# Kernel tuning notes

Measured on AMD Instinct MI355X. Metric: run time of the kernel, lower is better.

The kernel has to match this reference:

```python
import jax, jax.numpy as jnp
import numpy as np
import math

N, S, D, C, CLASSES = 512, 256, 512, 1024, 1000


def setup_inputs() -> dict:
    key = jax.random.key(0)
    ks = jax.random.split(key, 9)
    q = jax.random.normal(ks[0], (N, D), dtype=jnp.float32)
    K = jax.random.normal(ks[1], (N, S, D), dtype=jnp.float32)
    V = jax.random.normal(ks[2], (N, S, D), dtype=jnp.float32)
    codebook = jax.random.normal(ks[3], (C, D), dtype=jnp.float32) / math.sqrt(D)
    Wq = jax.random.normal(ks[4], (D, D), dtype=jnp.float32) / math.sqrt(D)
    Wc = jax.random.normal(ks[5], (CLASSES, D), dtype=jnp.float32) / math.sqrt(D)
    bc = jnp.zeros((CLASSES,), dtype=jnp.float32)
    Wr = jax.random.normal(ks[6], (D, D), dtype=jnp.float32) / math.sqrt(D)
    br = jnp.zeros((D,), dtype=jnp.float32)
    return {"q": q, "K": K, "V": V, "codebook": codebook,
            "Wq": Wq, "Wc": Wc, "bc": bc, "Wr": Wr, "br": br}


def reference(q, K, V, codebook, Wq, Wc, bc, Wr, br):
    d = q.shape[-1]
    scale = math.sqrt(d)
    # query projection (Linear, no bias): q @ Wq^T
    q_proj = jnp.einsum('nd,ed->ne', q, Wq)
    # query-to-codebook soft assignment [n, c]
    code_weights = jax.nn.softmax(jnp.einsum('nd,cd->nc', q_proj, codebook) / scale, axis=-1)
    # slot-to-codebook soft assignment [n, s, c]
    slot_code_weights = jax.nn.softmax(jnp.einsum('nsd,cd->nsc', K, codebook) / scale, axis=-1)
    # fused: einsum('nc,ncd->nd', code_weights, einsum('nsc,nsd->ncd', ...))
    # == contract c first to get per-slot weights [n, s], then mix V.
    effective_weights = jnp.einsum('nc,nsc->ns', code_weights, slot_code_weights)
    summary = jnp.einsum('ns,nsd->nd', effective_weights, V)
    logits = jnp.einsum('nd,kd->nk', summary, Wc) + bc
    recon = jnp.einsum('nd,ed->ne', summary, Wr) + br
    return (logits, recon, effective_weights)
```

## Files before the change

kernel.cpp:

```cpp
#include <hip/hip_runtime.h>
#include <hip/hip_bf16.h>
#include <stdint.h>


typedef float  f32x4 __attribute__((ext_vector_type(4)));
typedef float  f32x2 __attribute__((ext_vector_type(2)));
typedef short  s16x8 __attribute__((ext_vector_type(8)));

__device__ __forceinline__ unsigned short f2bf(float x){
  unsigned u = __float_as_uint(x);
  u += 0x7fffu + ((u >> 16) & 1u);
  return (unsigned short)(u >> 16);
}
__device__ __forceinline__ float hsum4(f32x4 v){ return v[0]+v[1]+v[2]+v[3]; }

static constexpr float INV_SCALE = 0.04419417382415922f;

__global__ __launch_bounds__(256) void k_prep(const float* __restrict__ cb,
                                              unsigned short* __restrict__ cbB,
                                              const float* __restrict__ q,
                                              const float* __restrict__ Wq,
                                              float* __restrict__ cw){
  __shared__ __align__(16) float qrow[2][512];
  __shared__ __align__(16) float qproj[2][512];
  __shared__ float ev[2][1024];
  __shared__ float red[256];
  __shared__ float tot[2];
  const int t = threadIdx.x;

  if (blockIdx.x < 256){
    const int g = blockIdx.x*256 + t;
    const int ks8 = g & 3;
    const int cr  = (g >> 2) & 31;
    const int kk  = (g >> 7) & 15;
    const int p   = g >> 11;
    const int c = p*32 + cr;
    const int k = kk*32 + ks8*8;
    const float* src = cb + (size_t)c*512 + k;
    const f32x4 v0 = *(const f32x4*)(src);
    const f32x4 v1 = *(const f32x4*)(src + 4);
    s16x8 o;
    o[0]=(short)f2bf(v0[0]*INV_SCALE); o[1]=(short)f2bf(v0[1]*INV_SCALE);
    o[2]=(short)f2bf(v0[2]*INV_SCALE); o[3]=(short)f2bf(v0[3]*INV_SCALE);
    o[4]=(short)f2bf(v1[0]*INV_SCALE); o[5]=(short)f2bf(v1[1]*INV_SCALE);
    o[6]=(short)f2bf(v1[2]*INV_SCALE); o[7]=(short)f2bf(v1[3]*INV_SCALE);
    *(s16x8*)(cbB + (size_t)g*8) = o;
    return;
  }

  const int n0 = (blockIdx.x - 256)*2;
  #pragma unroll
  for (int j = 0; j < 4; ++j){
    const int o = t + 256*j; const int ni = o >> 9, d = o & 511;
    qrow[ni][d] = q[(size_t)(n0+ni)*512 + d];
  }
  __syncthreads();
  {
    const f32x4* q0 = (const f32x4*)qrow[0];
    const f32x4* q1 = (const f32x4*)qrow[1];
    #pragma unroll 1
    for (int j = 0; j < 2; ++j){
      const int e = t + 256*j;
      const f32x4* w4 = (const f32x4*)(Wq + (size_t)e*512);
      f32x4 a0={0,0,0,0},a1={0,0,0,0};
      for (int d = 0; d < 128; ++d){
        const f32x4 wv = w4[d];
        a0 += wv*q0[d]; a1 += wv*q1[d];
      }
      qproj[0][e]=hsum4(a0); qproj[1][e]=hsum4(a1);
    }
  }
  __syncthreads();
  {
    const f32x4* p0 = (const f32x4*)qproj[0];
    const f32x4* p1 = (const f32x4*)qproj[1];
    #pragma unroll 1
    for (int j = 0; j < 4; ++j){
      const int c = t + 256*j;
      const f32x4* c4 = (const f32x4*)(cb + (size_t)c*512);
      f32x4 a0={0,0,0,0},a1={0,0,0,0};
      for (int d = 0; d < 128; ++d){
        const f32x4 wv = c4[d];
        a0 += wv*p0[d]; a1 += wv*p1[d];
      }
      ev[0][c] = __expf(hsum4(a0)*INV_SCALE);
      ev[1][c] = __expf(hsum4(a1)*INV_SCALE);
    }
  }
  __syncthreads();
  for (int ni = 0; ni < 2; ++ni){
    red[t] = ev[ni][t] + ev[ni][t+256] + ev[ni][t+512] + ev[ni][t+768];
    __syncthreads();
    for (int off = 128; off > 0; off >>= 1){
      if (t < off) red[t] += red[t+off];
      __syncthreads();
    }
    if (t == 0) tot[ni] = red[0];
    __syncthreads();
  }
  #pragma unroll
  for (int j = 0; j < 8; ++j){
    const int o = t + 256*j; const int ni = o >> 10, c = o & 1023;
    cw[(size_t)(n0+ni)*1024 + c] = ev[ni][c] / tot[ni];
  }
}

template<bool FUSE_V>
__global__ __launch_bounds__(512, 4) void k_scores(const float* __restrict__ Kt,
                                                   const unsigned short* __restrict__ cbB,
                                                   const float* __restrict__ cw,
                                                   float* __restrict__ ew_out,
                                                   const float* __restrict__ Vp,
                                                   float* __restrict__ partial){
  __shared__ __align__(16) short sA[64*512];
  __shared__ float cwl[1024];
  __shared__ float pe[8][64];
  __shared__ float pw[8][64];
  __shared__ float ewl[64];

  const int t    = threadIdx.x;
  const int lane = t & 63;
  const int w    = t >> 6;
  const int m0   = blockIdx.x * 64;
  const int n    = m0 >> 8;

  {
    const int row = t >> 3;
    const float* src = Kt + (size_t)(m0 + row) * 512;
    #pragma unroll
    for (int j = 0; j < 8; ++j){
      const int slot = (t & 7) + 8*j;
      const f32x4 v0 = *(const f32x4*)(src + slot*8);
      const f32x4 v1 = *(const f32x4*)(src + slot*8 + 4);
      s16x8 o;
      o[0]=(short)f2bf(v0[0]); o[1]=(short)f2bf(v0[1]); o[2]=(short)f2bf(v0[2]); o[3]=(short)f2bf(v0[3]);
      o[4]=(short)f2bf(v1[0]); o[5]=(short)f2bf(v1[1]); o[6]=(short)f2bf(v1[2]); o[7]=(short)f2bf(v1[3]);
      const int sp = slot ^ (row & 7);
      *(s16x8*)&sA[row*512 + sp*8] = o;
    }
  }
  cwl[t]       = cw[(size_t)n*1024 + t];
  cwl[t + 512] = cw[(size_t)n*1024 + t + 512];
  __syncthreads();

  const int kg = lane >> 4;
  const int lr = lane & 15;
  const int rot = blockIdx.x & 3;

  float es[4][4], ws[4][4];
  #pragma unroll
  for (int fr = 0; fr < 4; ++fr)
    #pragma unroll
    for (int r = 0; r < 4; ++r){ es[fr][r] = 0.f; ws[fr][r] = 0.f; }

  #pragma unroll 1
  for (int p = 0; p < 4; ++p){
    const int ci = (p + rot) & 3;
    f32x4 acc[4][2];
    #pragma unroll
    for (int fr = 0; fr < 4; ++fr)
      #pragma unroll
      for (int fc = 0; fc < 2; ++fc) acc[fr][fc] = (f32x4){0.f,0.f,0.f,0.f};

    const unsigned short* pbase = cbB + ((size_t)(ci*8 + w))*16384;
    const int loff = lr*32 + kg*8;

    s16x8 a[4], b[2][2];
    #pragma unroll
    for (int fc = 0; fc < 2; ++fc)
      b[0][fc] = *(const s16x8*)(pbase + 0*1024 + fc*512 + loff);
    #pragma unroll
    for (int fc = 0; fc < 2; ++fc)
      b[1][fc] = *(const s16x8*)(pbase + 1*1024 + fc*512 + loff);

    #pragma unroll
    for (int kk = 0; kk < 16; ++kk){
      if (kk < 15) asm volatile("s_waitcnt vmcnt(2)" ::: "memory");
      else         asm volatile("s_waitcnt vmcnt(0)" ::: "memory");
      __builtin_amdgcn_sched_barrier(0);
      #pragma unroll
      for (int fr = 0; fr < 4; ++fr){
        const int row = fr*16 + lr;
        const int sp  = (kk*4 + kg) ^ (row & 7);
        a[fr] = *(const s16x8*)&sA[row*512 + sp*8];
      }
      __builtin_amdgcn_s_setprio(1);
      #pragma unroll
      for (int fr = 0; fr < 4; ++fr)
        #pragma unroll
        for (int fc = 0; fc < 2; ++fc)
          acc[fr][fc] = __builtin_amdgcn_mfma_f32_16x16x32_bf16(a[fr], b[kk & 1][fc], acc[fr][fc], 0, 0, 0);
      __builtin_amdgcn_s_setprio(0);
      __builtin_amdgcn_sched_barrier(0);
      if (kk < 14){
        #pragma unroll
        for (int fc = 0; fc < 2; ++fc)
          b[kk & 1][fc] = *(const s16x8*)(pbase + (size_t)(kk+2)*1024 + fc*512 + loff);
      }
    }

    const float cwv0 = cwl[ci*256 + w*32 + 0*16 + lr];
    const float cwv1 = cwl[ci*256 + w*32 + 1*16 + lr];
    #pragma unroll
    for (int fr = 0; fr < 4; ++fr){
      #pragma unroll
      for (int r = 0; r < 4; ++r){
        const float e0 = __expf(acc[fr][0][r]);
        const float e1 = __expf(acc[fr][1][r]);
        es[fr][r] += e0 + e1;
        ws[fr][r] += e0 * cwv0 + e1 * cwv1;
      }
    }
  }

  #pragma unroll
  for (int fr = 0; fr < 4; ++fr){
    #pragma unroll
    for (int r = 0; r < 4; ++r){
      float a0 = es[fr][r], b0 = ws[fr][r];
      #pragma unroll
      for (int m = 1; m < 16; m <<= 1){
        a0 += __shfl_xor(a0, m, 64);
        b0 += __shfl_xor(b0, m, 64);
      }
      if (lr == 0){
        const int row = fr*16 + kg*4 + r;
        pe[w][row] = a0;
        pw[w][row] = b0;
      }
    }
  }

  __syncthreads();
  if (t < 64){
    float se = 0.f, sw = 0.f;
    #pragma unroll
    for (int i = 0; i < 8; ++i){ se += pe[i][t]; sw += pw[i][t]; }
    const float e = sw / se;
    ew_out[m0 + t] = e;
    ewl[t] = e;
  }

  if constexpr (FUSE_V){
    __syncthreads();
    float* psum = (float*)sA;
    const int sh = t >> 7;
    const int dq = (t & 127) * 4;
    const float* vb = Vp + (size_t)m0*512 + dq;
    f32x4 av = {0.f,0.f,0.f,0.f};
    #pragma unroll
    for (int i = 0; i < 16; ++i){
      const int s = sh*16 + i;
      av += ewl[s] * *(const f32x4*)(vb + (size_t)s*512);
    }
    *(f32x4*)&psum[sh*512 + dq] = av;
    __syncthreads();
    if (t < 128){
      const int d4 = t*4;
      f32x4 r = *(f32x4*)&psum[d4];
      r += *(f32x4*)&psum[512 + d4];
      r += *(f32x4*)&psum[1024 + d4];
      r += *(f32x4*)&psum[1536 + d4];
      *(f32x4*)&partial[(size_t)blockIdx.x*512 + d4] = r;
    }
  }
}

__global__ __launch_bounds__(256) void k_summary(const float* __restrict__ V,
                                                 const float* __restrict__ ew,
                                                 float* __restrict__ sm){
  __shared__ float e[256];
  __shared__ f32x4 red[3][64];
  const int t = threadIdx.x;
  const int lane = t & 63, w = t >> 6;
  const int n = blockIdx.x >> 1;
  const int d0 = (blockIdx.x & 1) * 256;
  e[t] = ew[(size_t)n*256 + t];
  __syncthreads();
  const float* vb = V + (size_t)n*131072 + d0 + lane*4;
  f32x4 acc = {0.f,0.f,0.f,0.f};
  #pragma unroll 8
  for (int s = w; s < 256; s += 4){
    const f32x4 v = *(const f32x4*)(vb + (size_t)s*512);
    acc += e[s] * v;
  }
  if (w > 0) red[w-1][lane] = acc;
  __syncthreads();
  if (w == 0){
    acc += red[0][lane] + red[1][lane] + red[2][lane];
    *(f32x4*)(sm + (size_t)n*512 + d0 + lane*4) = acc;
  }
}

template<bool FUSED>
__global__ __launch_bounds__(256) void k_readout(const float* __restrict__ src,
                                                 const float* __restrict__ Wc,
                                                 const float* __restrict__ bc,
                                                 const float* __restrict__ Wr,
                                                 const float* __restrict__ br,
                                                 float* __restrict__ logits,
                                                 float* __restrict__ recon){
  __shared__ __align__(16) float sl[8][512];
  const int t = threadIdx.x;
  const int nb  = blockIdx.x >> 2;
  const int wsl = blockIdx.x & 3;
  const int n0 = nb * 8;
  #pragma unroll
  for (int j = 0; j < 16; ++j){
    const int o = t + 256*j; const int ni = o >> 9, d = o & 511;
    if (FUSED){
      const float* pb = src + (size_t)(n0+ni)*2048 + d;
      sl[ni][d] = pb[0] + pb[512] + pb[1024] + pb[1536];
    } else {
      sl[ni][d] = src[(size_t)(n0+ni)*512 + d];
    }
  }
  __syncthreads();
  #pragma unroll 1
  for (int j = 0; j < 2; ++j){
    const int rel = t + 256*j;
    if (rel >= 378) continue;
    const int o = wsl*378 + rel;
    const bool isl = o < 1000;
    const float* wrow = isl ? (Wc + (size_t)o*512) : (Wr + (size_t)(o-1000)*512);
    const float bias  = isl ? bc[o] : br[o-1000];
    const f32x4* w4 = (const f32x4*)wrow;
    f32x4 av[8];
    #pragma unroll
    for (int ni = 0; ni < 8; ++ni) av[ni] = (f32x4){0.f,0.f,0.f,0.f};
    for (int d = 0; d < 128; ++d){
      const f32x4 wv = w4[d];
      #pragma unroll
      for (int ni = 0; ni < 8; ++ni)
        av[ni] += wv * ((const f32x4*)sl[ni])[d];
    }
    #pragma unroll
    for (int ni = 0; ni < 8; ++ni){
      const float r = hsum4(av[ni]) + bias;
      if (isl) logits[(size_t)(n0+ni)*1000 + o] = r;
      else     recon [(size_t)(n0+ni)*512 + (o-1000)] = r;
    }
  }
}

extern "C" void kernel_launch(void* const* d_in, const int* in_sizes, int n_in,
                              void* d_out, int out_size, void* d_ws, size_t ws_size,
                              hipStream_t stream) {
  const float* q  = (const float*)d_in[0];
  const float* K  = (const float*)d_in[1];
  const float* V  = (const float*)d_in[2];
  const float* cb = (const float*)d_in[3];
  const float* Wq = (const float*)d_in[4];
  const float* Wc = (const float*)d_in[5];
  const float* bc = (const float*)d_in[6];
  const float* Wr = (const float*)d_in[7];
  const float* br = (const float*)d_in[8];

  float* out    = (float*)d_out;
  float* logits = out;
  float* recon  = out + 512*1000;
  float* ew     = out + 512*1000 + 512*512;

  char* wsb = (char*)d_ws;
  unsigned short* cbB = (unsigned short*)wsb;
  float* cw   = (float*)(wsb + (1u<<20));
  float* aux  = (float*)(wsb + 3u*(1u<<20));

  const bool fused = ws_size >= (size_t)(7u<<20);

  k_prep<<<dim3(512), dim3(256), 0, stream>>>(cb, cbB, q, Wq, cw);
  if (fused){
    k_scores<true><<<dim3(2048), dim3(512), 0, stream>>>(K, cbB, cw, ew, V, aux);
    k_readout<true><<<dim3(256), dim3(256), 0, stream>>>(aux, Wc, bc, Wr, br, logits, recon);
  } else {
    k_scores<false><<<dim3(2048), dim3(512), 0, stream>>>(K, cbB, cw, ew, V, aux);
    k_summary<<<dim3(1024), dim3(256), 0, stream>>>(V, ew, aux);
    k_readout<false><<<dim3(256), dim3(256), 0, stream>>>(aux, Wc, bc, Wr, br, logits, recon);
  }
}
```

Before: 372.6 us.

## Double-step codebook K loop with per-wave rotated K order and per-pass reductions

The inner K loop of the slot-codebook MFMA now processes two K-steps per iteration, with four B fragments in flight instead of two. Each wave starts at a different K offset, rotated by its wave index, presumably to spread global and LDS access across banks and channels. The exp-sum accumulators are no longer held in registers across passes. Each pass reduces with shuffles and accumulates into shared pe/pw, which are zeroed at the start. This lowers register pressure and raises memory-level parallelism, at the cost of 4x more shuffle reductions and extra shared-memory read-modify-writes.

```diff
diff --git a/kernel.cpp b/kernel.cpp
--- a/kernel.cpp
+++ b/kernel.cpp
@@ -141,17 +141,13 @@
   }
   cwl[t]       = cw[(size_t)n*1024 + t];
   cwl[t + 512] = cw[(size_t)n*1024 + t + 512];
+  pe[w][lane] = 0.f;
+  pw[w][lane] = 0.f;
   __syncthreads();
 
   const int kg = lane >> 4;
   const int lr = lane & 15;
   const int rot = blockIdx.x & 3;
-
-  float es[4][4], ws[4][4];
-  #pragma unroll
-  for (int fr = 0; fr < 4; ++fr)
-    #pragma unroll
-    for (int r = 0; r < 4; ++r){ es[fr][r] = 0.f; ws[fr][r] = 0.f; }
 
   #pragma unroll 1
   for (int p = 0; p < 4; ++p){
@@ -165,37 +161,49 @@
     const unsigned short* pbase = cbB + ((size_t)(ci*8 + w))*16384;
     const int loff = lr*32 + kg*8;
 
-    s16x8 a[4], b[2][2];
-    #pragma unroll
-    for (int fc = 0; fc < 2; ++fc)
-      b[0][fc] = *(const s16x8*)(pbase + 0*1024 + fc*512 + loff);
-    #pragma unroll
-    for (int fc = 0; fc < 2; ++fc)
-      b[1][fc] = *(const s16x8*)(pbase + 1*1024 + fc*512 + loff);
-
-    #pragma unroll
-    for (int kk = 0; kk < 16; ++kk){
-      if (kk < 15) asm volatile("s_waitcnt vmcnt(2)" ::: "memory");
-      else         asm volatile("s_waitcnt vmcnt(0)" ::: "memory");
+    s16x8 a[2][4], b[4][2];
+    #pragma unroll
+    for (int s = 0; s < 2; ++s){
+      const int kb = (((s + w) & 7)) * 2;
+      #pragma unroll
+      for (int u = 0; u < 2; ++u)
+        #pragma unroll
+        for (int fc = 0; fc < 2; ++fc)
+          b[2*s + u][fc] = *(const s16x8*)(pbase + (size_t)(kb + u)*1024 + fc*512 + loff);
+    }
+
+    #pragma unroll
+    for (int jj = 0; jj < 8; ++jj){
+      const int kk0 = (((jj + w) & 7)) * 2;
+      if (jj < 7) asm volatile("s_waitcnt vmcnt(4)" ::: "memory");
+      else        asm volatile("s_waitcnt vmcnt(0)" ::: "memory");
       __builtin_amdgcn_sched_barrier(0);
       #pragma unroll
-      for (int fr = 0; fr < 4; ++fr){
-        const int row = fr*16 + lr;
-        const int sp  = (kk*4 + kg) ^ (row & 7);
-        a[fr] = *(const s16x8*)&sA[row*512 + sp*8];
-      }
+      for (int u = 0; u < 2; ++u)
+        #pragma unroll
+        for (int fr = 0; fr < 4; ++fr){
+          const int row = fr*16 + lr;
+          const int sp  = ((kk0 + u)*4 + kg) ^ (row & 7);
+          a[u][fr] = *(const s16x8*)&sA[row*512 + sp*8];
+        }
+      const int base = (jj & 1) * 2;
       __builtin_amdgcn_s_setprio(1);
       #pragma unroll
-      for (int fr = 0; fr < 4; ++fr)
-        #pragma unroll
-        for (int fc = 0; fc < 2; ++fc)
-          acc[fr][fc] = __builtin_amdgcn_mfma_f32_16x16x32_bf16(a[fr], b[kk & 1][fc], acc[fr][fc], 0, 0, 0);
+      for (int u = 0; u < 2; ++u)
+        #pragma unroll
+        for (int fr = 0; fr < 4; ++fr)
+          #pragma unroll
+          for (int fc = 0; fc < 2; ++fc)
+            acc[fr][fc] = __builtin_amdgcn_mfma_f32_16x16x32_bf16(a[u][fr], b[base + u][fc], acc[fr][fc], 0, 0, 0);
       __builtin_amdgcn_s_setprio(0);
       __builtin_amdgcn_sched_barrier(0);
-      if (kk < 14){
-        #pragma unroll
-        for (int fc = 0; fc < 2; ++fc)
-          b[kk & 1][fc] = *(const s16x8*)(pbase + (size_t)(kk+2)*1024 + fc*512 + loff);
+      if (jj < 6){
+        const int kn = (((jj + 2 + w) & 7)) * 2;
+        #pragma unroll
+        for (int u = 0; u < 2; ++u)
+          #pragma unroll
+          for (int fc = 0; fc < 2; ++fc)
+            b[base + u][fc] = *(const s16x8*)(pbase + (size_t)(kn + u)*1024 + fc*512 + loff);
       }
     }
 
@@ -203,30 +211,27 @@
     const float cwv1 = cwl[ci*256 + w*32 + 1*16 + lr];
     #pragma unroll
     for (int fr = 0; fr < 4; ++fr){
+      float es[4], ws[4];
       #pragma unroll
       for (int r = 0; r < 4; ++r){
         const float e0 = __expf(acc[fr][0][r]);
         const float e1 = __expf(acc[fr][1][r]);
-        es[fr][r] += e0 + e1;
-        ws[fr][r] += e0 * cwv0 + e1 * cwv1;
-      }
-    }
-  }
-
-  #pragma unroll
-  for (int fr = 0; fr < 4; ++fr){
-    #pragma unroll
-    for (int r = 0; r < 4; ++r){
-      float a0 = es[fr][r], b0 = ws[fr][r];
-      #pragma unroll
-      for (int m = 1; m < 16; m <<= 1){
-        a0 += __shfl_xor(a0, m, 64);
-        b0 += __shfl_xor(b0, m, 64);
-      }
-      if (lr == 0){
-        const int row = fr*16 + kg*4 + r;
-        pe[w][row] = a0;
-        pw[w][row] = b0;
+        es[r] = e0 + e1;
+        ws[r] = e0 * cwv0 + e1 * cwv1;
+      }
+      #pragma unroll
+      for (int r = 0; r < 4; ++r){
+        float a0 = es[r], b0 = ws[r];
+        #pragma unroll
+        for (int m = 1; m < 16; m <<= 1){
+          a0 += __shfl_xor(a0, m, 64);
+          b0 += __shfl_xor(b0, m, 64);
+        }
+        if (lr == 0){
+          const int row = fr*16 + kg*4 + r;
+          pe[w][row] += a0;
+          pw[w][row] += b0;
+        }
       }
     }
   }
```

After: 423.8 us. +13.7%, slower.
